# Performance work log

Measured on AMD Instinct MI355X. Metric: run time of the kernel, lower is better.

Reference implementation:

```python
import jax, jax.numpy as jnp
import numpy as np

S = (256, 256, 256)          # MRI volume shape
N = 50000                    # number of Gaussians
T = 16                       # fixed tile edge; covers max bbox width = 2*3*sigma_max*(S-1)+2 <= 15
SIG_MIN, SIG_MAX = 0.004, 0.008  # NN-distance-based sigma range (k_sigma=1)


def setup_inputs() -> dict:
    key = jax.random.key(0)
    k1, k2, k3 = jax.random.split(key, 3)
    centers = jax.random.uniform(k1, (N, 3), dtype=jnp.float32)
    sigmas = jax.random.uniform(k2, (N,), dtype=jnp.float32, minval=SIG_MIN, maxval=SIG_MAX)
    intensities = jax.random.uniform(k3, (N,), dtype=jnp.float32)
    return {"centers": centers, "sigmas": sigmas, "intensities": intensities}


def _splat(centers, sigmas, intensities):
    dt = centers.dtype
    scale = jnp.asarray([s - 1 for s in S], dtype=dt)            # (3,) == scale_factors
    shape_f = jnp.asarray(S, dtype=dt)                           # (3,)
    shape_i = jnp.asarray(S, dtype=jnp.int32)                    # (3,)

    center_vox = centers * scale                                 # (N,3) voxel-space centers
    cutoff = 3.0 * sigmas[:, None] * scale                       # (N,3)
    # original: min_idx = max(c-cut, 0).int(); max_idx = (min(c+cut, scale)+1).int(), clipped to S
    min_idx = jnp.floor(jnp.maximum(center_vox - cutoff, 0.0)).astype(jnp.int32)          # (N,3)
    max_idx = jnp.minimum(jnp.floor(jnp.minimum(center_vox + cutoff, scale)) + 1.0,
                          shape_f).astype(jnp.int32)             # (N,3), exclusive

    ar = jnp.arange(T, dtype=jnp.int32)
    idx = min_idx[:, :, None] + ar[None, None, :]                # (N,3,T) absolute voxel idx
    valid = idx < max_idx[:, :, None]                            # (N,3,T) inside variable bbox
    idx_c = jnp.minimum(idx, shape_i[None, :, None] - 1)         # clamp for safe gather/scatter

    # grid coordinate along axis a at voxel i is i/(S_a-1) (linspace(0,1,S_a))
    coord = idx_c.astype(dt) / scale[None, :, None]              # (N,3,T)
    d = coord - centers[:, :, None]                              # (N,3,T)
    d2 = (d[:, 0, :, None, None] ** 2
          + d[:, 1, None, :, None] ** 2
          + d[:, 2, None, None, :] ** 2)                         # (N,T,T,T)
    mask = (valid[:, 0, :, None, None]
            & valid[:, 1, None, :, None]
            & valid[:, 2, None, None, :])                        # (N,T,T,T)

    inv_two_sig2 = 0.5 / (sigmas * sigmas)                       # (N,)
    contrib = intensities[:, None, None, None] * jnp.exp(-d2 * inv_two_sig2[:, None, None, None])
    contrib = jnp.where(mask, contrib, jnp.zeros((), dt))        # (N,T,T,T)

    lin = (idx_c[:, 0, :, None, None] * (S[1] * S[2])
           + idx_c[:, 1, None, :, None] * S[2]
           + idx_c[:, 2, None, None, :])                         # (N,T,T,T) flat voxel index

    vol = jnp.zeros(S[0] * S[1] * S[2], dtype=dt)
    vol = vol.at[lin.reshape(-1)].add(contrib.reshape(-1))
    return vol.reshape(S)


def reference(centers, sigmas, intensities):
    return _splat(centers, sigmas, intensities)
```

## Files before the change

kernel.cpp:

```cpp
#include <hip/hip_runtime.h>


#define NTILE 32768
#define CAP   32
#define LOG2E 1.4426950408889634f

typedef unsigned long long ull;

struct __align__(16) Rec {
    float cy, cz, w2;
    unsigned meta;
    float ex[8];
};

__global__ __launch_bounds__(256) void bin_prep_kernel(
    const float* __restrict__ centers,
    const float* __restrict__ sigmas,
    const float* __restrict__ intens,
    int*  __restrict__ counts,
    Rec*  __restrict__ list,
    int N)
{
    int g = blockIdx.x * 256 + threadIdx.x;
    if (g >= N) return;
    int txi = blockIdx.y % 3;
    int tyi = blockIdx.y / 3;

    float cx = centers[3*g+0] * 255.0f;
    float cy = centers[3*g+1] * 255.0f;
    float cz = centers[3*g+2] * 255.0f;
    float sig = sigmas[g];
    float cut = 3.0f * sig * 255.0f;
    float cc[3] = {cx, cy, cz};
    int mn[3], mx[3];
    #pragma unroll
    for (int a = 0; a < 3; ++a) {
        mn[a] = (int)floorf(fmaxf(cc[a] - cut, 0.0f));
        mx[a] = (int)fminf(floorf(fminf(cc[a] + cut, 255.0f)) + 1.0f, 256.0f);
    }
    float s255 = sig * 255.0f;
    float w2 = -0.5f * LOG2E / (s255 * s255);
    float inten = intens[g];

    int t0x = mn[0] >> 3, t1x = (mx[0] - 1) >> 3;
    int t0y = mn[1] >> 3, t1y = (mx[1] - 1) >> 3;

    int tx = t0x + txi; if (tx > t1x) return;
    int ty = t0y + tyi; if (ty > t1y) return;

    int ox = tx << 3, oy = ty << 3;
    int lox = max(mn[0] - ox, 0), hix = min(mx[0] - ox, 8);
    int loy = max(mn[1] - oy, 0), hiy = min(mx[1] - oy, 8);

    float ex[8];
    #pragma unroll
    for (int i = 0; i < 8; ++i) {
        float d = (float)(ox + i) - cx;
        float v = exp2f(d * d * w2) * inten;
        ex[i] = (i >= lox && i < hix) ? v : 0.0f;
    }

    int tzc = ((int)cz) >> 3;
    int t = (tx << 10) | (ty << 5) | tzc;
    unsigned meta = (unsigned)mn[2] | ((unsigned)(mx[2] - 1) << 8)
                  | ((unsigned)loy << 16) | ((unsigned)hiy << 19);

    int slot = atomicAdd(&counts[t], 1);
    if (slot < CAP) {
        int4* p = (int4*)&list[(size_t)t * CAP + slot];
        p[0] = make_int4(__float_as_int(cy), __float_as_int(cz),
                         __float_as_int(w2), (int)meta);
        p[1] = make_int4(__float_as_int(ex[0]), __float_as_int(ex[1]),
                         __float_as_int(ex[2]), __float_as_int(ex[3]));
        p[2] = make_int4(__float_as_int(ex[4]), __float_as_int(ex[5]),
                         __float_as_int(ex[6]), __float_as_int(ex[7]));
    }
}

__global__ __launch_bounds__(256) void splat_main(
    const int*  __restrict__ counts,
    const Rec*  __restrict__ list,
    float* __restrict__ vol)
{
    int wid = threadIdx.x >> 6;
    int lane = threadIdx.x & 63;
    int t = __builtin_amdgcn_readfirstlane(blockIdx.x * 4 + wid);
    int ox = (t >> 10) << 3, oy = ((t >> 5) & 31) << 3, oz = (t & 31) << 3;
    int tz = t & 31;
    int ly = lane >> 3, lz = lane & 7;

    int c0 = (tz > 0)  ? counts[t - 1] : 0;  if (c0 > CAP) c0 = CAP;
    int c1 = counts[t];                       if (c1 > CAP) c1 = CAP;
    int c2 = (tz < 31) ? counts[t + 1] : 0;  if (c2 > CAP) c2 = CAP;
    int e1 = c0 + c1, ntot = e1 + c2;

    const int4* sA = (const int4*)(list + (long)(t - 1) * CAP);
    const int4* sB = (const int4*)(list + (long)t * CAP);
    const int4* sC = (const int4*)(list + (long)(t + 1) * CAP);

    int4 A0, A1, A2;
    auto load_rec = [&](int r) {
        const int4* src; int rr;
        if (r < c0)        { src = sA; rr = r; }
        else if (r < e1)   { src = sB; rr = r - c0; }
        else if (r < ntot) { src = sC; rr = r - e1; }
        else               { src = sB; rr = 0; }
        A0 = src[rr * 3]; A1 = src[rr * 3 + 1]; A2 = src[rr * 3 + 2];
    };

    float fy = (float)(oy + ly);
    float fz = (float)(oz + lz);

    float acc[8];
    #pragma unroll
    for (int i = 0; i < 8; ++i) acc[i] = 0.0f;

    auto body = [&](int k) {
        unsigned meta = (unsigned)__builtin_amdgcn_readlane(A0.w, k);
        int mnz  = (int)(meta & 0xFF);
        int mxzi = (int)((meta >> 8) & 0xFF);
        int loz = mnz - oz;      if (loz < 0) loz = 0;
        int hiz = mxzi + 1 - oz; if (hiz > 8) hiz = 8;
        if (loz < hiz) {
            int loy_ = (int)((meta >> 16) & 7);
            int hiy_ = (int)((meta >> 19) & 0xF);
            ull ym = ((~0ull) << (loy_ << 3)) & ((~0ull) >> (64 - (hiy_ << 3)));
            unsigned zpat = (0xFFu >> (8 - hiz)) & (0xFFu << loz);
            unsigned zrep = zpat * 0x01010101u;
            ull m = (((ull)zrep << 32) | (ull)zrep) & ym;

            float cyv = __int_as_float(__builtin_amdgcn_readlane(A0.x, k));
            float czv = __int_as_float(__builtin_amdgcn_readlane(A0.y, k));
            float w2v = __int_as_float(__builtin_amdgcn_readlane(A0.z, k));

            float dy = fy - cyv, dz = fz - czv;
            float e = exp2f(fmaf(dy, dy, dz * dz) * w2v);
            float em;
            asm("v_cndmask_b32 %0, 0, %1, %2" : "=v"(em) : "v"(e), "s"(m));

            float ex0 = __int_as_float(__builtin_amdgcn_readlane(A1.x, k));
            float ex1 = __int_as_float(__builtin_amdgcn_readlane(A1.y, k));
            float ex2 = __int_as_float(__builtin_amdgcn_readlane(A1.z, k));
            float ex3 = __int_as_float(__builtin_amdgcn_readlane(A1.w, k));
            float ex4 = __int_as_float(__builtin_amdgcn_readlane(A2.x, k));
            float ex5 = __int_as_float(__builtin_amdgcn_readlane(A2.y, k));
            float ex6 = __int_as_float(__builtin_amdgcn_readlane(A2.z, k));
            float ex7 = __int_as_float(__builtin_amdgcn_readlane(A2.w, k));

            acc[0] = fmaf(ex0, em, acc[0]);
            acc[1] = fmaf(ex1, em, acc[1]);
            acc[2] = fmaf(ex2, em, acc[2]);
            acc[3] = fmaf(ex3, em, acc[3]);
            acc[4] = fmaf(ex4, em, acc[4]);
            acc[5] = fmaf(ex5, em, acc[5]);
            acc[6] = fmaf(ex6, em, acc[6]);
            acc[7] = fmaf(ex7, em, acc[7]);
        }
    };

    load_rec(lane);
    int n1 = ntot < 64 ? ntot : 64;
    for (int k = 0; k < n1; ++k) body(k);
    if (ntot > 64) {
        load_rec(lane + 64);
        int n2 = ntot - 64;
        for (int k = 0; k < n2; ++k) body(k);
    }

    int ybase = ((oy + ly) << 8) + (oz + lz);
    #pragma unroll
    for (int i = 0; i < 8; ++i)
        vol[((ox + i) << 16) + ybase] = acc[i];
}

extern "C" void kernel_launch(void* const* d_in, const int* in_sizes, int n_in,
                              void* d_out, int out_size, void* d_ws, size_t ws_size,
                              hipStream_t stream) {
    const float* centers = (const float*)d_in[0];
    const float* sigmas  = (const float*)d_in[1];
    const float* intens  = (const float*)d_in[2];
    float* vol = (float*)d_out;
    const int N = in_sizes[1];

    char* ws = (char*)d_ws;
    int*  counts = (int*)ws;
    Rec*  list   = (Rec*)(ws + (size_t)NTILE * sizeof(int));

    hipMemsetAsync(counts, 0, (size_t)NTILE * sizeof(int), stream);

    int gblocks = (N + 255) / 256;
    bin_prep_kernel<<<dim3(gblocks, 9), 256, 0, stream>>>(centers, sigmas, intens,
                                                          counts, list, N);
    splat_main<<<NTILE / 4, 256, 0, stream>>>(counts, list, vol);
}
```

Baseline: 133.2 us.

## Split tile records into geometry and extent arrays, prefetch geometry as scalars

Splits each per-tile Gaussian record into a geometry array (cy, cz, w2, meta) and a separate x-extent array. In the main loop the geometry is read through wave-uniform loads with a six-deep software prefetch, replacing four readlane operations per Gaussian with scalar loads. The exp2f calls are swapped for raw v_exp_f32 inline assembly. This adds scalar memory traffic and register pressure, and prefetches may read past the valid records, which relies on the added padding.

```diff
diff --git a/kernel.cpp b/kernel.cpp
--- a/kernel.cpp
+++ b/kernel.cpp
@@ -7,18 +7,19 @@
 
 typedef unsigned long long ull;
 
-struct __align__(16) Rec {
-    float cy, cz, w2;
-    unsigned meta;
-    float ex[8];
-};
+__device__ __forceinline__ float fast_exp2(float x) {
+    float r;
+    asm("v_exp_f32 %0, %1" : "=v"(r) : "v"(x));
+    return r;
+}
 
 __global__ __launch_bounds__(256) void bin_prep_kernel(
     const float* __restrict__ centers,
     const float* __restrict__ sigmas,
     const float* __restrict__ intens,
     int*  __restrict__ counts,
-    Rec*  __restrict__ list,
+    int4* __restrict__ geoL,
+    int4* __restrict__ exL,
     int N)
 {
     int g = blockIdx.x * 256 + threadIdx.x;
@@ -56,7 +57,7 @@
     #pragma unroll
     for (int i = 0; i < 8; ++i) {
         float d = (float)(ox + i) - cx;
-        float v = exp2f(d * d * w2) * inten;
+        float v = fast_exp2(d * d * w2) * inten;
         ex[i] = (i >= lox && i < hix) ? v : 0.0f;
     }
 
@@ -67,19 +68,20 @@
 
     int slot = atomicAdd(&counts[t], 1);
     if (slot < CAP) {
-        int4* p = (int4*)&list[(size_t)t * CAP + slot];
-        p[0] = make_int4(__float_as_int(cy), __float_as_int(cz),
-                         __float_as_int(w2), (int)meta);
-        p[1] = make_int4(__float_as_int(ex[0]), __float_as_int(ex[1]),
-                         __float_as_int(ex[2]), __float_as_int(ex[3]));
-        p[2] = make_int4(__float_as_int(ex[4]), __float_as_int(ex[5]),
-                         __float_as_int(ex[6]), __float_as_int(ex[7]));
+        int gi = t * CAP + slot;
+        geoL[gi] = make_int4(__float_as_int(cy), __float_as_int(cz),
+                             __float_as_int(w2), (int)meta);
+        exL[2*gi]   = make_int4(__float_as_int(ex[0]), __float_as_int(ex[1]),
+                                __float_as_int(ex[2]), __float_as_int(ex[3]));
+        exL[2*gi+1] = make_int4(__float_as_int(ex[4]), __float_as_int(ex[5]),
+                                __float_as_int(ex[6]), __float_as_int(ex[7]));
     }
 }
 
 __global__ __launch_bounds__(256) void splat_main(
     const int*  __restrict__ counts,
-    const Rec*  __restrict__ list,
+    const int4* __restrict__ geoL,
+    const int4* __restrict__ exL,
     float* __restrict__ vol)
 {
     int wid = threadIdx.x >> 6;
@@ -89,24 +91,27 @@
     int tz = t & 31;
     int ly = lane >> 3, lz = lane & 7;
 
-    int c0 = (tz > 0)  ? counts[t - 1] : 0;  if (c0 > CAP) c0 = CAP;
-    int c1 = counts[t];                       if (c1 > CAP) c1 = CAP;
-    int c2 = (tz < 31) ? counts[t + 1] : 0;  if (c2 > CAP) c2 = CAP;
+    int c0 = (tz > 0)  ? __builtin_amdgcn_readfirstlane(counts[t - 1]) : 0;
+    if (c0 > CAP) c0 = CAP;
+    int c1 = __builtin_amdgcn_readfirstlane(counts[t]);
+    if (c1 > CAP) c1 = CAP;
+    int c2 = (tz < 31) ? __builtin_amdgcn_readfirstlane(counts[t + 1]) : 0;
+    if (c2 > CAP) c2 = CAP;
     int e1 = c0 + c1, ntot = e1 + c2;
 
-    const int4* sA = (const int4*)(list + (long)(t - 1) * CAP);
-    const int4* sB = (const int4*)(list + (long)t * CAP);
-    const int4* sC = (const int4*)(list + (long)(t + 1) * CAP);
-
-    int4 A0, A1, A2;
-    auto load_rec = [&](int r) {
-        const int4* src; int rr;
-        if (r < c0)        { src = sA; rr = r; }
-        else if (r < e1)   { src = sB; rr = r - c0; }
-        else if (r < ntot) { src = sC; rr = r - e1; }
-        else               { src = sB; rr = 0; }
-        A0 = src[rr * 3]; A1 = src[rr * 3 + 1]; A2 = src[rr * 3 + 2];
+    int gbase = (t - 1) * CAP;
+    auto gidx = [&](int r) -> int {
+        int a = (r >= c0) ? (CAP - c0) : 0;
+        int b = (r >= e1) ? (CAP - c1) : 0;
+        return gbase + r + a + b;
     };
+
+    int4 EX0, EX1;
+    auto load_ex = [&](int r) {
+        int gi = (r < ntot) ? gidx(r) : (t * CAP);
+        EX0 = exL[2*gi]; EX1 = exL[2*gi+1];
+    };
+    load_ex(lane);
 
     float fy = (float)(oy + ly);
     float fz = (float)(oz + lz);
@@ -115,8 +120,8 @@
     #pragma unroll
     for (int i = 0; i < 8; ++i) acc[i] = 0.0f;
 
-    auto body = [&](int k) {
-        unsigned meta = (unsigned)__builtin_amdgcn_readlane(A0.w, k);
+    auto body = [&](int kk, int4 g) {
+        unsigned meta = (unsigned)__builtin_amdgcn_readfirstlane(g.w);
         int mnz  = (int)(meta & 0xFF);
         int mxzi = (int)((meta >> 8) & 0xFF);
         int loz = mnz - oz;      if (loz < 0) loz = 0;
@@ -129,23 +134,23 @@
             unsigned zrep = zpat * 0x01010101u;
             ull m = (((ull)zrep << 32) | (ull)zrep) & ym;
 
-            float cyv = __int_as_float(__builtin_amdgcn_readlane(A0.x, k));
-            float czv = __int_as_float(__builtin_amdgcn_readlane(A0.y, k));
-            float w2v = __int_as_float(__builtin_amdgcn_readlane(A0.z, k));
+            float cyv = __int_as_float(g.x);
+            float czv = __int_as_float(g.y);
+            float w2v = __int_as_float(g.z);
 
             float dy = fy - cyv, dz = fz - czv;
-            float e = exp2f(fmaf(dy, dy, dz * dz) * w2v);
+            float e = fast_exp2(fmaf(dy, dy, dz * dz) * w2v);
             float em;
             asm("v_cndmask_b32 %0, 0, %1, %2" : "=v"(em) : "v"(e), "s"(m));
 
-            float ex0 = __int_as_float(__builtin_amdgcn_readlane(A1.x, k));
-            float ex1 = __int_as_float(__builtin_amdgcn_readlane(A1.y, k));
-            float ex2 = __int_as_float(__builtin_amdgcn_readlane(A1.z, k));
-            float ex3 = __int_as_float(__builtin_amdgcn_readlane(A1.w, k));
-            float ex4 = __int_as_float(__builtin_amdgcn_readlane(A2.x, k));
-            float ex5 = __int_as_float(__builtin_amdgcn_readlane(A2.y, k));
-            float ex6 = __int_as_float(__builtin_amdgcn_readlane(A2.z, k));
-            float ex7 = __int_as_float(__builtin_amdgcn_readlane(A2.w, k));
+            float ex0 = __int_as_float(__builtin_amdgcn_readlane(EX0.x, kk));
+            float ex1 = __int_as_float(__builtin_amdgcn_readlane(EX0.y, kk));
+            float ex2 = __int_as_float(__builtin_amdgcn_readlane(EX0.z, kk));
+            float ex3 = __int_as_float(__builtin_amdgcn_readlane(EX0.w, kk));
+            float ex4 = __int_as_float(__builtin_amdgcn_readlane(EX1.x, kk));
+            float ex5 = __int_as_float(__builtin_amdgcn_readlane(EX1.y, kk));
+            float ex6 = __int_as_float(__builtin_amdgcn_readlane(EX1.z, kk));
+            float ex7 = __int_as_float(__builtin_amdgcn_readlane(EX1.w, kk));
 
             acc[0] = fmaf(ex0, em, acc[0]);
             acc[1] = fmaf(ex1, em, acc[1]);
@@ -158,13 +163,22 @@
         }
     };
 
-    load_rec(lane);
+    int4 g0 = geoL[gidx(0)], g1 = geoL[gidx(1)], g2 = geoL[gidx(2)];
+    int4 g3 = geoL[gidx(3)], g4 = geoL[gidx(4)], g5 = geoL[gidx(5)];
     int n1 = ntot < 64 ? ntot : 64;
-    for (int k = 0; k < n1; ++k) body(k);
+    int k = 0;
+    for (; k < n1; ++k) {
+        int4 gn = geoL[gidx(k + 6)];
+        body(k, g0);
+        g0 = g1; g1 = g2; g2 = g3; g3 = g4; g4 = g5; g5 = gn;
+    }
     if (ntot > 64) {
-        load_rec(lane + 64);
-        int n2 = ntot - 64;
-        for (int k = 0; k < n2; ++k) body(k);
+        load_ex(lane + 64);
+        for (; k < ntot; ++k) {
+            int4 gn = geoL[gidx(k + 6)];
+            body(k - 64, g0);
+            g0 = g1; g1 = g2; g2 = g3; g3 = g4; g4 = g5; g5 = gn;
+        }
     }
 
     int ybase = ((oy + ly) << 8) + (oz + lz);
@@ -184,12 +198,14 @@
 
     char* ws = (char*)d_ws;
     int*  counts = (int*)ws;
-    Rec*  list   = (Rec*)(ws + (size_t)NTILE * sizeof(int));
-
-    hipMemsetAsync(counts, 0, (size_t)NTILE * sizeof(int), stream);
+    int4* geoL   = (int4*)(ws + (size_t)NTILE * sizeof(int));
+    int4* exL    = (int4*)(ws + (size_t)NTILE * sizeof(int)
+                              + ((size_t)NTILE * CAP + 128) * 16);
+
+    (void)hipMemsetAsync(counts, 0, (size_t)NTILE * sizeof(int), stream);
 
     int gblocks = (N + 255) / 256;
     bin_prep_kernel<<<dim3(gblocks, 9), 256, 0, stream>>>(centers, sigmas, intens,
-                                                          counts, list, N);
-    splat_main<<<NTILE / 4, 256, 0, stream>>>(counts, list, vol);
-}
+                                                          counts, geoL, exL, N);
+    splat_main<<<NTILE / 4, 256, 0, stream>>>(counts, geoL, exL, vol);
+}
```

New measurement: 144.9 us. 1.09x slower.
